# Optimization experiments

Hardware: AMD Instinct MI355X
Metric: run time of the kernel (lower is better)

## Reference

```python
import jax, jax.numpy as jnp
import numpy as np

B, L, D_NODE, D_EDGE, H = 4, 256, 256, 128, 8
DK = D_NODE // H        # 32, per-head node dim
DE = D_EDGE // H        # 16, per-head edge dim
NEG_SLOPE = 0.2

# Static index maps replicating the torch loop indexing (including its j-1 off-by-one / wraparound bug)
_GIDX = np.arange(L - 1)[None, :] + (np.arange(L - 1)[None, :] >= np.arange(L)[:, None])  # [L, L-1]: j-values visited for row i (j != i, in order)
_PIDX = (np.arange(L) - 1) % (L - 1)   # [L]: torch uses attention_probs[:, j-1] for every j != i
_II = np.arange(L)[:, None]            # [L, 1]


def lrelu(x):
    return jnp.where(x >= 0, x, NEG_SLOPE * x)


def setup_inputs() -> dict:
    key = jax.random.key(0)
    ks = jax.random.split(key, 19)
    w = lambda k, s, sc=0.05: jax.random.normal(k, s, jnp.float32) * sc
    return dict(
        node=w(ks[0], (B, L, D_NODE), 1.0),
        edge=w(ks[1], (B, L, L, D_EDGE), 1.0),
        Wn_w=w(ks[2], (D_NODE, D_NODE)), Wn_b=w(ks[3], (D_NODE,)),
        Wh_w=w(ks[4], (DK, DK)), Wh_b=w(ks[5], (DK,)),
        We_w=w(ks[6], (D_EDGE, D_EDGE)), We_b=w(ks[7], (D_EDGE,)),
        Wn2_w=w(ks[8], (D_NODE, D_NODE)), Wn2_b=w(ks[9], (D_NODE,)),
        We2_w=w(ks[10], (D_EDGE, D_EDGE)), We2_b=w(ks[11], (D_EDGE,)),
        attn_w=w(ks[12], (2 * DK + DE,)),                  # attn_linear (no bias), input order [hi, hj, eij]
        edge_w=w(ks[13], (DE + 2 * DK, DE)), edge_b=w(ks[14], (DE,)),  # edge_linear, input order [eij, hi, hj]
        out_n_w=w(ks[15], (D_NODE, D_NODE)), out_n_b=w(ks[16], (D_NODE,)),
        out_e_w=w(ks[17], (D_EDGE, D_EDGE)), out_e_b=w(ks[18], (D_EDGE,)),
    )


def reference(node, edge, Wn_w, Wn_b, Wh_w, Wh_b, We_w, We_b, Wn2_w, Wn2_b,
              We2_w, We2_b, attn_w, edge_w, edge_b, out_n_w, out_n_b, out_e_w, out_e_b):
    node_p = (node @ Wn_w + Wn_b).reshape(B, L, H, DK)
    edge_p = (edge @ We_w + We_b).reshape(B, L, L, H, DE)

    # ---- node update (all heads at once) ----
    wq, wk, we = attn_w[:DK], attn_w[DK:2 * DK], attn_w[2 * DK:]
    si = jnp.einsum('bihd,d->bih', node_p, wq)
    sj = jnp.einsum('bjhd,d->bjh', node_p, wk)
    se = jnp.einsum('bijhd,d->bijh', edge_p, we)
    scores = si[:, :, None, :] + sj[:, None, :, :] + se          # [B,L,L,H], score(i,j)
    sc = scores[:, _II, _GIDX, :]                                 # [B,L,L-1,H]: j != i, loop order
    probs = jax.nn.softmax(lrelu(sc), axis=2)                     # softmax over the L-1 neighbors
    probs_pair = probs[:, :, _PIDX, :]                            # [B,L,L,H]: replicate probs[:, j-1]
    mask = (1.0 - jnp.eye(L, dtype=node.dtype))[None, :, :, None]
    Whh = jnp.einsum('bjhd,de->bjhe', node_p, Wh_w) + Wh_b        # Wh(hj), bias inside the sum
    agg = jnp.einsum('bijh,bjhe->bihe', probs_pair * mask, Whh)
    node_h = (node_p + lrelu(agg)).reshape(B, L, D_NODE)          # concat heads == reshape
    new_node = node_h @ out_n_w + out_n_b

    # ---- edge update ----
    node_p2 = (new_node @ Wn2_w + Wn2_b).reshape(B, L, H, DK)
    edge_p2 = (edge @ We2_w + We2_b).reshape(B, L, L, H, DE)
    w_e, w_i, w_j = edge_w[:DE], edge_w[DE:DE + DK], edge_w[DE + DK:]
    e_new = (jnp.einsum('bijhd,de->bijhe', edge_p2, w_e)
             + jnp.einsum('bihd,de->bihe', node_p2, w_i)[:, :, None]
             + jnp.einsum('bjhd,de->bjhe', node_p2, w_j)[:, None]
             + edge_b)
    e_new = e_new * mask[..., None]                               # diagonal stays zero (zeros_like init)
    new_edge = e_new.reshape(B, L, L, D_EDGE) @ out_e_w + out_e_b
    return new_node, new_edge
```

## Files before the change

### kernel.cpp

```cpp
#include <hip/hip_runtime.h>

#define Bb 4
#define Ll 256
#define NEG 0.2f

typedef __attribute__((ext_vector_type(8))) short short8;
typedef __attribute__((ext_vector_type(4))) float f32x4;
typedef __attribute__((ext_vector_type(4))) unsigned uint4v;

__device__ __forceinline__ float lrelu(float x) { return x >= 0.f ? x : NEG * x; }

__device__ __forceinline__ short f2bf(float x) {
  unsigned u = __builtin_bit_cast(unsigned, x);
  unsigned r = (u + 0x7FFFu + ((u >> 16) & 1u)) >> 16;
  return (short)r;
}

__device__ __forceinline__ unsigned pack2bf(float e, float o) {
  unsigned ue = __builtin_bit_cast(unsigned, e);
  unsigned uo = __builtin_bit_cast(unsigned, o);
  return ((ue + 0x8000u) >> 16) | ((uo + 0x8000u) & 0xFFFF0000u);
}

__global__ void prep_kernel(const float* We_w, const float* We_b, const float* attn_w,
                            const float* We2_w, const float* We2_b, const float* edge_w,
                            const float* edge_b, const float* out_e_w, const float* out_e_b,
                            float* Vg, float* chg, float* c0g, short* Gt) {
  int blk = blockIdx.x;
  int t = threadIdx.x;
  if (blk < 128) {
    __shared__ float m2[128];
    int c = blk;
    int h = t >> 4, e = t & 15;
    float s = 0.f;
    for (int d = 0; d < 16; ++d) s += We2_w[c * 128 + h * 16 + d] * edge_w[d * 16 + e];
    m2[t] = s;
    __syncthreads();
    float g = 0.f;
    for (int f = 0; f < 128; ++f) g += m2[f] * out_e_w[f * 128 + t];
    Gt[t * 128 + c] = f2bf(g);
  } else {
    __shared__ float b2e[128];
    const float* we = attn_w + 64;
    for (int idx = t; idx < 1024; idx += 128) {
      int c = idx >> 3, h = idx & 7;
      float s = 0.f;
      for (int d = 0; d < 16; ++d) s += We_w[c * 128 + h * 16 + d] * we[d];
      Vg[idx] = s;
    }
    if (t < 8) {
      float s = 0.f;
      for (int d = 0; d < 16; ++d) s += We_b[t * 16 + d] * we[d];
      chg[t] = s;
    }
    {
      int h = t >> 4, e = t & 15;
      float s = 0.f;
      for (int d = 0; d < 16; ++d) s += We2_b[h * 16 + d] * edge_w[d * 16 + e];
      b2e[t] = s + edge_b[e];
    }
    __syncthreads();
    float s = out_e_b[t];
    for (int f = 0; f < 128; ++f) s += b2e[f] * out_e_w[f * 128 + t];
    c0g[t] = s;
  }
}

__global__ __launch_bounds__(256) void node_in_fused(
    const float* __restrict__ node, const float* __restrict__ Wn_w,
    const float* __restrict__ Wn_b, const float* __restrict__ Wh_w,
    const float* __restrict__ Wh_b, const float* __restrict__ attn_w,
    float* __restrict__ node_p, float* __restrict__ Whh, float* __restrict__ si,
    float* __restrict__ sj) {
  __shared__ float a[4][256];
  __shared__ float np[4][256];
  int t = threadIdx.x;
  int row0 = blockIdx.x * 4;
  for (int q = t; q < 1024; q += 256) a[q >> 8][q & 255] = node[(long)row0 * 256 + q];
  __syncthreads();
  float acc[4];
  float bvv = Wn_b[t];
#pragma unroll
  for (int r = 0; r < 4; ++r) acc[r] = bvv;
  for (int k = 0; k < 256; ++k) {
    float w = Wn_w[k * 256 + t];
#pragma unroll
    for (int r = 0; r < 4; ++r) acc[r] += a[r][k] * w;
  }
#pragma unroll
  for (int r = 0; r < 4; ++r) {
    node_p[(long)(row0 + r) * 256 + t] = acc[r];
    np[r][t] = acc[r];
  }
  __syncthreads();
  int h = t >> 5, e = t & 31;
  float wb2 = Wh_b[e];
#pragma unroll
  for (int r = 0; r < 4; ++r) {
    float s = wb2;
    for (int d = 0; d < 32; ++d) s += np[r][h * 32 + d] * Wh_w[d * 32 + e];
    Whh[(long)(row0 + r) * 256 + t] = s;
  }
  if (t < 64) {
    int r = t >> 4, idx = t & 15, hh = idx & 7;
    const float* w = attn_w + (idx < 8 ? 0 : 32);
    float s = 0.f;
    for (int d = 0; d < 32; ++d) s += np[r][hh * 32 + d] * w[d];
    ((idx < 8) ? si : sj)[(long)(row0 + r) * 8 + hh] = s;
  }
}

__global__ __launch_bounds__(256) void attn_fused(
    const float* __restrict__ node_p, const float* __restrict__ Whh,
    const float* __restrict__ si, const float* __restrict__ sj,
    const float* __restrict__ edge, const float* __restrict__ Vg,
    const float* __restrict__ chg, float* __restrict__ node_h) {
  __shared__ float sjl[2048];
  __shared__ float sel[2048];
  __shared__ float pl[2048];
  __shared__ float sil[8];
  int t = threadIdx.x, bi = blockIdx.x;
  int b = bi >> 8, i = bi & 255;
  for (int q = t; q < 2048; q += 256) sjl[q] = sj[(long)b * 2048 + q];
  if (t < 8) sil[t] = si[(long)bi * 8 + t];

  int l16 = t & 15, grp = t >> 4;
  float vreg[8][8];
#pragma unroll
  for (int ci = 0; ci < 8; ++ci) {
    int c = (ci < 4) ? (l16 * 4 + ci) : (64 + l16 * 4 + (ci - 4));
#pragma unroll
    for (int h = 0; h < 8; ++h) vreg[ci][h] = Vg[c * 8 + h];
  }
  float chv = chg[(l16 >> 1) & 7];
  const float4* eb = reinterpret_cast<const float4*>(edge + (long)bi * 32768);
#pragma unroll 2
  for (int it = 0; it < 16; ++it) {
    int j = it * 16 + grp;
    float4 e0 = eb[j * 32 + l16];
    float4 e1 = eb[j * 32 + 16 + l16];
    float p[8];
#pragma unroll
    for (int h = 0; h < 8; ++h)
      p[h] = e0.x * vreg[0][h] + e0.y * vreg[1][h] + e0.z * vreg[2][h] + e0.w * vreg[3][h] +
             e1.x * vreg[4][h] + e1.y * vreg[5][h] + e1.z * vreg[6][h] + e1.w * vreg[7][h];
    bool hi8 = (l16 & 8) != 0;
    float q[4];
#pragma unroll
    for (int h = 0; h < 4; ++h) {
      float keep = hi8 ? p[h + 4] : p[h];
      float send = hi8 ? p[h] : p[h + 4];
      q[h] = keep + __shfl_xor(send, 8);
    }
    bool hi4 = (l16 & 4) != 0;
    float r2[2];
#pragma unroll
    for (int h = 0; h < 2; ++h) {
      float keep = hi4 ? q[h + 2] : q[h];
      float send = hi4 ? q[h] : q[h + 2];
      r2[h] = keep + __shfl_xor(send, 4);
    }
    bool hi2 = (l16 & 2) != 0;
    float s = (hi2 ? r2[1] : r2[0]) + __shfl_xor(hi2 ? r2[0] : r2[1], 2);
    s += __shfl_xor(s, 1);
    s += chv;
    if ((l16 & 1) == 0) sel[j * 8 + (l16 >> 1)] = s;
  }
  __syncthreads();

  int g = t >> 5, l32 = t & 31;
  float sc[8];
  float mx = -1e30f;
#pragma unroll
  for (int m = 0; m < 8; ++m) {
    int k = l32 + 32 * m;
    float v = -1e30f;
    if (k < 255) {
      int jj = k + (k >= i ? 1 : 0);
      v = sil[g] + sjl[jj * 8 + g] + sel[jj * 8 + g];
      v = lrelu(v);
    }
    sc[m] = v;
    mx = fmaxf(mx, v);
  }
#pragma unroll
  for (int d = 16; d >= 1; d >>= 1) mx = fmaxf(mx, __shfl_xor(mx, d));
  float sum = 0.f;
#pragma unroll
  for (int m = 0; m < 8; ++m) {
    int k = l32 + 32 * m;
    float e = (k < 255) ? __expf(sc[m] - mx) : 0.f;
    sc[m] = e;
    sum += e;
  }
#pragma unroll
  for (int d = 16; d >= 1; d >>= 1) sum += __shfl_xor(sum, d);
  float inv = 1.f / sum;
#pragma unroll
  for (int m = 0; m < 8; ++m) {
    int k = l32 + 32 * m;
    if (k < 255) pl[k * 8 + g] = sc[m] * inv;
  }
  __syncthreads();

  int h = g;
  const float* wb = Whh + (long)b * 65536 + t;
  float acc0 = 0.f, acc1 = 0.f;
#pragma unroll 4
  for (int j = 0; j < 256; j += 2) {
    int k0 = (j == 0) ? 254 : (j - 1);
    int k1 = j;
    float w0 = (j == i) ? 0.f : pl[k0 * 8 + h];
    float w1 = (j + 1 == i) ? 0.f : pl[k1 * 8 + h];
    acc0 += w0 * wb[(long)j * 256];
    acc1 += w1 * wb[(long)(j + 1) * 256];
  }
  float acc = acc0 + acc1;
  float np = node_p[(long)bi * 256 + t];
  node_h[(long)bi * 256 + t] = np + lrelu(acc);
}

__global__ __launch_bounds__(256) void node_out_pq(
    const float* __restrict__ node_h, const float* __restrict__ out_n_w,
    const float* __restrict__ out_n_b, const float* __restrict__ Wn2_w,
    const float* __restrict__ Wn2_b, const float* __restrict__ edge_w,
    const float* __restrict__ out_e_w, float* __restrict__ out_node,
    float* __restrict__ Pg, float* __restrict__ Qg) {
  __shared__ float a[4][256];
  __shared__ float b2[4][256];
  __shared__ float ninj[4][256];
  int t = threadIdx.x;
  int row0 = blockIdx.x * 4;
  for (int q = t; q < 1024; q += 256) a[q >> 8][q & 255] = node_h[(long)row0 * 256 + q];
  __syncthreads();
  float acc[4];
  float bv1 = out_n_b[t];
#pragma unroll
  for (int r = 0; r < 4; ++r) acc[r] = bv1;
  for (int k = 0; k < 256; ++k) {
    float w = out_n_w[k * 256 + t];
#pragma unroll
    for (int r = 0; r < 4; ++r) acc[r] += a[r][k] * w;
  }
#pragma unroll
  for (int r = 0; r < 4; ++r) {
    out_node[(long)(row0 + r) * 256 + t] = acc[r];
    b2[r][t] = acc[r];
  }
  __syncthreads();
  float acc2[4];
  float bv2 = Wn2_b[t];
#pragma unroll
  for (int r = 0; r < 4; ++r) acc2[r] = bv2;
  for (int k = 0; k < 256; ++k) {
    float w = Wn2_w[k * 256 + t];
#pragma unroll
    for (int r = 0; r < 4; ++r) acc2[r] += b2[r][k] * w;
  }
#pragma unroll
  for (int r = 0; r < 4; ++r) a[r][t] = acc2[r];
  __syncthreads();
  {
    int f = t & 127, h = f >> 4, e = f & 15;
    const float* w = edge_w + 256 + (t >> 7) * 512;
#pragma unroll
    for (int r = 0; r < 4; ++r) {
      float s = 0.f;
      for (int d = 0; d < 32; ++d) s += a[r][h * 32 + d] * w[d * 16 + e];
      ninj[r][t] = s;
    }
  }
  __syncthreads();
  {
    int o = t & 127;
    int half = (t >> 7) * 128;
#pragma unroll
    for (int r = 0; r < 4; ++r) {
      float s = 0.f;
      const float* src = ninj[r] + half;
      for (int f = 0; f < 128; ++f) s += src[f] * out_e_w[f * 128 + o];
      ((t < 128) ? Pg : Qg)[(long)(row0 + r) * 128 + o] = s;
    }
  }
}

__global__ __launch_bounds__(256, 2) void edge_out_kernel(
    const float* __restrict__ edge, const short* __restrict__ Gt,
    const float* __restrict__ Pg, const float* __restrict__ Qg,
    const float* __restrict__ c0g, const float* __restrict__ oeb,
    float* __restrict__ out_edge) {
  int t = threadIdx.x;
  int l = t & 63, wid = t >> 6;
  int wm = wid >> 1, wn = wid & 1;
  int lc = l & 15, lq = l >> 4;

  long row0 = (long)blockIdx.x * 128;
  int b = (int)(row0 >> 16);
  int i = (int)((row0 >> 8) & 255);
  int j0 = (int)(row0 & 255);

  short8 bv[4][4];
#pragma unroll
  for (int ks = 0; ks < 4; ++ks)
#pragma unroll
    for (int nf = 0; nf < 4; ++nf)
      bv[ks][nf] = *(const short8*)(Gt + (wn * 64 + nf * 16 + lc) * 128 + ks * 32 + lq * 8);

  f32x4 acc[4][4];
#pragma unroll
  for (int mf = 0; mf < 4; ++mf)
#pragma unroll
    for (int nf = 0; nf < 4; ++nf) acc[mf][nf] = (f32x4){0.f, 0.f, 0.f, 0.f};

  const float* ebase = edge + row0 * 128;
#pragma unroll
  for (int ks = 0; ks < 4; ++ks) {
    short8 av[4];
#pragma unroll
    for (int mf = 0; mf < 4; ++mf) {
      const float* ap = ebase + (long)(wm * 64 + mf * 16 + lc) * 128 + ks * 32 + lq * 8;
      float4 f0 = *(const float4*)ap;
      float4 f1 = *(const float4*)(ap + 4);
      uint4v u;
      u.x = pack2bf(f0.x, f0.y);
      u.y = pack2bf(f0.z, f0.w);
      u.z = pack2bf(f1.x, f1.y);
      u.w = pack2bf(f1.z, f1.w);
      av[mf] = __builtin_bit_cast(short8, u);
    }
#pragma unroll
    for (int mf = 0; mf < 4; ++mf)
#pragma unroll
      for (int nf = 0; nf < 4; ++nf)
        acc[mf][nf] =
            __builtin_amdgcn_mfma_f32_16x16x32_bf16(bv[ks][nf], av[mf], acc[mf][nf], 0, 0, 0);
  }

  f32x4 pc[4];
#pragma unroll
  for (int nf = 0; nf < 4; ++nf) {
    int cb = wn * 64 + nf * 16 + lq * 4;
    f32x4 p = *(const f32x4*)(Pg + ((long)(b * 256 + i)) * 128 + cb);
    f32x4 c0 = *(const f32x4*)(c0g + cb);
    pc[nf] = p + c0;
  }
#pragma unroll
  for (int mf = 0; mf < 4; ++mf) {
    int er = wm * 64 + mf * 16 + lc;
    int j = j0 + er;
    const float* Qrow = Qg + ((long)(b * 256 + j)) * 128;
    float* orow = out_edge + (row0 + er) * 128;
    if (j == i) {
#pragma unroll
      for (int nf = 0; nf < 4; ++nf) {
        int cb = wn * 64 + nf * 16 + lq * 4;
        *(f32x4*)(orow + cb) = *(const f32x4*)(oeb + cb);
      }
    } else {
#pragma unroll
      for (int nf = 0; nf < 4; ++nf) {
        int cb = wn * 64 + nf * 16 + lq * 4;
        f32x4 q4 = *(const f32x4*)(Qrow + cb);
        *(f32x4*)(orow + cb) = acc[mf][nf] + pc[nf] + q4;
      }
    }
  }
}

extern "C" void kernel_launch(void* const* d_in, const int* in_sizes, int n_in,
                              void* d_out, int out_size, void* d_ws, size_t ws_size,
                              hipStream_t stream) {
  const float* node = (const float*)d_in[0];
  const float* edge = (const float*)d_in[1];
  const float* Wn_w = (const float*)d_in[2];
  const float* Wn_b = (const float*)d_in[3];
  const float* Wh_w = (const float*)d_in[4];
  const float* Wh_b = (const float*)d_in[5];
  const float* We_w = (const float*)d_in[6];
  const float* We_b = (const float*)d_in[7];
  const float* Wn2_w = (const float*)d_in[8];
  const float* Wn2_b = (const float*)d_in[9];
  const float* We2_w = (const float*)d_in[10];
  const float* We2_b = (const float*)d_in[11];
  const float* attn_w = (const float*)d_in[12];
  const float* edge_w = (const float*)d_in[13];
  const float* edge_b = (const float*)d_in[14];
  const float* out_n_w = (const float*)d_in[15];
  const float* out_n_b = (const float*)d_in[16];
  const float* out_e_w = (const float*)d_in[17];
  const float* out_e_b = (const float*)d_in[18];

  float* out_node = (float*)d_out;
  float* out_edge = ((float*)d_out) + 262144;

  float* ws = (float*)d_ws;
  float* node_p = ws;
  float* Whh    = ws + 262144;
  float* node_h = ws + 524288;
  float* si     = ws + 786432;
  float* sjv    = ws + 794624;
  float* Pg     = ws + 802816;
  float* Qg     = ws + 933888;
  float* Vg     = ws + 1064960;
  float* chg    = ws + 1065984;
  short* Gt     = (short*)(ws + 1066112);
  float* c0g    = ws + 1074304;

  prep_kernel<<<129, 128, 0, stream>>>(We_w, We_b, attn_w, We2_w, We2_b, edge_w, edge_b,
                                       out_e_w, out_e_b, Vg, chg, c0g, Gt);
  node_in_fused<<<256, 256, 0, stream>>>(node, Wn_w, Wn_b, Wh_w, Wh_b, attn_w, node_p, Whh,
                                         si, sjv);
  attn_fused<<<1024, 256, 0, stream>>>(node_p, Whh, si, sjv, edge, Vg, chg, node_h);
  node_out_pq<<<256, 256, 0, stream>>>(node_h, out_n_w, out_n_b, Wn2_w, Wn2_b, edge_w,
                                       out_e_w, out_node, Pg, Qg);
  edge_out_kernel<<<2048, 256, 0, stream>>>(edge, Gt, Pg, Qg, c0g, out_e_b, out_edge);
}
```

Before: 173.3 us.

## Split edge score into MFMA pass that caches bf16 edge copy for output GEMM

Moves the per-edge attention score projection out of attn_fused into a separate pass_a kernel that computes it with bf16 MFMA and writes per-slab scores to workspace. When the workspace is large enough, pass_a also writes a bf16 copy of the edge tensor, so edge_out_kernel reads half the bytes instead of re-reading and converting fp32 edge. This trades a 32 MB bf16 write plus an extra kernel launch for a smaller read in the final GEMM and a simpler attention kernel. It also raises the unroll of the aggregation loop and drops the launch-bounds occupancy hint on edge_out. Scores now use bf16 inputs, which lowers precision.

```diff
diff --git a/kernel.cpp b/kernel.cpp
--- a/kernel.cpp
+++ b/kernel.cpp
@@ -25,7 +25,7 @@
 __global__ void prep_kernel(const float* We_w, const float* We_b, const float* attn_w,
                             const float* We2_w, const float* We2_b, const float* edge_w,
                             const float* edge_b, const float* out_e_w, const float* out_e_b,
-                            float* Vg, float* chg, float* c0g, short* Gt) {
+                            short* Vbf, float* chg, float* c0g, short* Gt) {
   int blk = blockIdx.x;
   int t = threadIdx.x;
   if (blk < 128) {
@@ -46,7 +46,8 @@
       int c = idx >> 3, h = idx & 7;
       float s = 0.f;
       for (int d = 0; d < 16; ++d) s += We_w[c * 128 + h * 16 + d] * we[d];
-      Vg[idx] = s;
+      Vbf[h * 128 + c] = f2bf(s);
+      Vbf[(h + 8) * 128 + c] = 0;
     }
     if (t < 8) {
       float s = 0.f;
@@ -63,6 +64,59 @@
     float s = out_e_b[t];
     for (int f = 0; f < 128; ++f) s += b2e[f] * out_e_w[f * 128 + t];
     c0g[t] = s;
+  }
+}
+
+template <bool WE>
+__global__ __launch_bounds__(256) void pass_a(const float* __restrict__ edge,
+                                              const short* __restrict__ Vbf,
+                                              const float* __restrict__ chg,
+                                              short* __restrict__ ebf,
+                                              float* __restrict__ seg) {
+  int t = threadIdx.x;
+  int l = t & 63, w = t >> 6;
+  int lc = l & 15, lq = l >> 4;
+  long slab = blockIdx.x;
+  const float* ebase = edge + slab * 32768;
+
+  short8 vb[4];
+#pragma unroll
+  for (int ks = 0; ks < 4; ++ks) vb[ks] = *(const short8*)(Vbf + lc * 128 + ks * 32 + lq * 8);
+
+  f32x4 acc[4];
+#pragma unroll
+  for (int mf = 0; mf < 4; ++mf) acc[mf] = (f32x4){0.f, 0.f, 0.f, 0.f};
+
+#pragma unroll
+  for (int mf = 0; mf < 4; ++mf) {
+    int row = w * 64 + mf * 16 + lc;
+    const float* ap = ebase + row * 128 + lq * 8;
+    float4 f[8];
+#pragma unroll
+    for (int ks = 0; ks < 4; ++ks) {
+      f[2 * ks] = *(const float4*)(ap + ks * 32);
+      f[2 * ks + 1] = *(const float4*)(ap + ks * 32 + 4);
+    }
+#pragma unroll
+    for (int ks = 0; ks < 4; ++ks) {
+      uint4v u;
+      u.x = pack2bf(f[2 * ks].x, f[2 * ks].y);
+      u.y = pack2bf(f[2 * ks].z, f[2 * ks].w);
+      u.z = pack2bf(f[2 * ks + 1].x, f[2 * ks + 1].y);
+      u.w = pack2bf(f[2 * ks + 1].z, f[2 * ks + 1].w);
+      if constexpr (WE) *(uint4v*)(ebf + slab * 32768 + row * 128 + ks * 32 + lq * 8) = u;
+      acc[mf] = __builtin_amdgcn_mfma_f32_16x16x32_bf16(vb[ks], __builtin_bit_cast(short8, u),
+                                                        acc[mf], 0, 0, 0);
+    }
+  }
+  if (lq < 2) {
+    f32x4 chv = *(const f32x4*)(chg + lq * 4);
+#pragma unroll
+    for (int mf = 0; mf < 4; ++mf) {
+      int row = w * 64 + mf * 16 + lc;
+      f32x4 v = acc[mf] + chv;
+      *(f32x4*)(seg + slab * 2048 + row * 8 + lq * 4) = v;
+    }
   }
 }
 
@@ -113,8 +167,7 @@
 __global__ __launch_bounds__(256) void attn_fused(
     const float* __restrict__ node_p, const float* __restrict__ Whh,
     const float* __restrict__ si, const float* __restrict__ sj,
-    const float* __restrict__ edge, const float* __restrict__ Vg,
-    const float* __restrict__ chg, float* __restrict__ node_h) {
+    const float* __restrict__ seg, float* __restrict__ node_h) {
   __shared__ float sjl[2048];
   __shared__ float sel[2048];
   __shared__ float pl[2048];
@@ -122,50 +175,8 @@
   int t = threadIdx.x, bi = blockIdx.x;
   int b = bi >> 8, i = bi & 255;
   for (int q = t; q < 2048; q += 256) sjl[q] = sj[(long)b * 2048 + q];
+  for (int q = t; q < 2048; q += 256) sel[q] = seg[(long)bi * 2048 + q];
   if (t < 8) sil[t] = si[(long)bi * 8 + t];
-
-  int l16 = t & 15, grp = t >> 4;
-  float vreg[8][8];
-#pragma unroll
-  for (int ci = 0; ci < 8; ++ci) {
-    int c = (ci < 4) ? (l16 * 4 + ci) : (64 + l16 * 4 + (ci - 4));
-#pragma unroll
-    for (int h = 0; h < 8; ++h) vreg[ci][h] = Vg[c * 8 + h];
-  }
-  float chv = chg[(l16 >> 1) & 7];
-  const float4* eb = reinterpret_cast<const float4*>(edge + (long)bi * 32768);
-#pragma unroll 2
-  for (int it = 0; it < 16; ++it) {
-    int j = it * 16 + grp;
-    float4 e0 = eb[j * 32 + l16];
-    float4 e1 = eb[j * 32 + 16 + l16];
-    float p[8];
-#pragma unroll
-    for (int h = 0; h < 8; ++h)
-      p[h] = e0.x * vreg[0][h] + e0.y * vreg[1][h] + e0.z * vreg[2][h] + e0.w * vreg[3][h] +
-             e1.x * vreg[4][h] + e1.y * vreg[5][h] + e1.z * vreg[6][h] + e1.w * vreg[7][h];
-    bool hi8 = (l16 & 8) != 0;
-    float q[4];
-#pragma unroll
-    for (int h = 0; h < 4; ++h) {
-      float keep = hi8 ? p[h + 4] : p[h];
-      float send = hi8 ? p[h] : p[h + 4];
-      q[h] = keep + __shfl_xor(send, 8);
-    }
-    bool hi4 = (l16 & 4) != 0;
-    float r2[2];
-#pragma unroll
-    for (int h = 0; h < 2; ++h) {
-      float keep = hi4 ? q[h + 2] : q[h];
-      float send = hi4 ? q[h] : q[h + 2];
-      r2[h] = keep + __shfl_xor(send, 4);
-    }
-    bool hi2 = (l16 & 2) != 0;
-    float s = (hi2 ? r2[1] : r2[0]) + __shfl_xor(hi2 ? r2[0] : r2[1], 2);
-    s += __shfl_xor(s, 1);
-    s += chv;
-    if ((l16 & 1) == 0) sel[j * 8 + (l16 >> 1)] = s;
-  }
   __syncthreads();
 
   int g = t >> 5, l32 = t & 31;
@@ -206,7 +217,7 @@
   int h = g;
   const float* wb = Whh + (long)b * 65536 + t;
   float acc0 = 0.f, acc1 = 0.f;
-#pragma unroll 4
+#pragma unroll 8
   for (int j = 0; j < 256; j += 2) {
     int k0 = (j == 0) ? 254 : (j - 1);
     int k1 = j;
@@ -284,11 +295,12 @@
   }
 }
 
-__global__ __launch_bounds__(256, 2) void edge_out_kernel(
-    const float* __restrict__ edge, const short* __restrict__ Gt,
-    const float* __restrict__ Pg, const float* __restrict__ Qg,
-    const float* __restrict__ c0g, const float* __restrict__ oeb,
-    float* __restrict__ out_edge) {
+template <bool UE>
+__global__ __launch_bounds__(256) void edge_out_kernel(
+    const float* __restrict__ edge, const short* __restrict__ ebf,
+    const short* __restrict__ Gt, const float* __restrict__ Pg,
+    const float* __restrict__ Qg, const float* __restrict__ c0g,
+    const float* __restrict__ oeb, float* __restrict__ out_edge) {
   int t = threadIdx.x;
   int l = t & 63, wid = t >> 6;
   int wm = wid >> 1, wn = wid & 1;
@@ -312,21 +324,25 @@
 #pragma unroll
     for (int nf = 0; nf < 4; ++nf) acc[mf][nf] = (f32x4){0.f, 0.f, 0.f, 0.f};
 
-  const float* ebase = edge + row0 * 128;
 #pragma unroll
   for (int ks = 0; ks < 4; ++ks) {
     short8 av[4];
 #pragma unroll
     for (int mf = 0; mf < 4; ++mf) {
-      const float* ap = ebase + (long)(wm * 64 + mf * 16 + lc) * 128 + ks * 32 + lq * 8;
-      float4 f0 = *(const float4*)ap;
-      float4 f1 = *(const float4*)(ap + 4);
-      uint4v u;
-      u.x = pack2bf(f0.x, f0.y);
-      u.y = pack2bf(f0.z, f0.w);
-      u.z = pack2bf(f1.x, f1.y);
-      u.w = pack2bf(f1.z, f1.w);
-      av[mf] = __builtin_bit_cast(short8, u);
+      long row = row0 + wm * 64 + mf * 16 + lc;
+      if constexpr (UE) {
+        av[mf] = *(const short8*)(ebf + row * 128 + ks * 32 + lq * 8);
+      } else {
+        const float* ap = edge + row * 128 + ks * 32 + lq * 8;
+        float4 f0 = *(const float4*)ap;
+        float4 f1 = *(const float4*)(ap + 4);
+        uint4v u;
+        u.x = pack2bf(f0.x, f0.y);
+        u.y = pack2bf(f0.z, f0.w);
+        u.z = pack2bf(f1.x, f1.y);
+        u.w = pack2bf(f1.z, f1.w);
+        av[mf] = __builtin_bit_cast(short8, u);
+      }
     }
 #pragma unroll
     for (int mf = 0; mf < 4; ++mf)
@@ -401,17 +417,29 @@
   float* sjv    = ws + 794624;
   float* Pg     = ws + 802816;
   float* Qg     = ws + 933888;
-  float* Vg     = ws + 1064960;
-  float* chg    = ws + 1065984;
-  short* Gt     = (short*)(ws + 1066112);
-  float* c0g    = ws + 1074304;
+  float* chg    = ws + 1064960;
+  float* c0g    = ws + 1065088;
+  short* Gt     = (short*)(ws + 1065216);
+  short* Vbf    = (short*)(ws + 1073408);
+  float* seg    = ws + 1074432;
+  short* ebf    = (short*)(ws + 3171584);
+  const bool big = ws_size >= (size_t)19948800 * 4;
 
   prep_kernel<<<129, 128, 0, stream>>>(We_w, We_b, attn_w, We2_w, We2_b, edge_w, edge_b,
-                                       out_e_w, out_e_b, Vg, chg, c0g, Gt);
+                                       out_e_w, out_e_b, Vbf, chg, c0g, Gt);
   node_in_fused<<<256, 256, 0, stream>>>(node, Wn_w, Wn_b, Wh_w, Wh_b, attn_w, node_p, Whh,
                                          si, sjv);
-  attn_fused<<<1024, 256, 0, stream>>>(node_p, Whh, si, sjv, edge, Vg, chg, node_h);
+  if (big)
+    pass_a<true><<<1024, 256, 0, stream>>>(edge, Vbf, chg, ebf, seg);
+  else
+    pass_a<false><<<1024, 256, 0, stream>>>(edge, Vbf, chg, ebf, seg);
+  attn_fused<<<1024, 256, 0, stream>>>(node_p, Whh, si, sjv, seg, node_h);
   node_out_pq<<<256, 256, 0, stream>>>(node_h, out_n_w, out_n_b, Wn2_w, Wn2_b, edge_w,
                                        out_e_w, out_node, Pg, Qg);
-  edge_out_kernel<<<2048, 256, 0, stream>>>(edge, Gt, Pg, Qg, c0g, out_e_b, out_edge);
-}
+  if (big)
+    edge_out_kernel<true><<<2048, 256, 0, stream>>>(edge, ebf, Gt, Pg, Qg, c0g, out_e_b,
+                                                    out_edge);
+  else
+    edge_out_kernel<false><<<2048, 256, 0, stream>>>(edge, ebf, Gt, Pg, Qg, c0g, out_e_b,
+                                                     out_edge);
+}
```

After: 193.5 us. 1.12x slower.
